# Performance work log

Hardware: AMD Instinct MI355X
Metric: run time of the kernel (lower is better)

Reference implementation:

```python
import jax, jax.numpy as jnp
import numpy as np

B, S, H, E = 4, 4096, 2048, 16
ED = H // 4
LN_EPS = 1e-5
ROUTING_SCALE = 0.01
NEG_INF = -1e9


def setup_inputs() -> dict:
    key = jax.random.key(0)
    ks = jax.random.split(key, 10)
    std = 0.02
    w_std = 1.0 / np.sqrt(H)  # roughly nn.Linear default scale
    return {
        "hidden_states": jax.random.normal(ks[0], (B, S, H), jnp.float32),
        "layer_embeddings": jax.random.normal(ks[1], (E, H), jnp.float32) * std,
        "centrality_embeddings": jax.random.normal(ks[2], (E, H), jnp.float32) * std,
        "spatial_embeddings": jax.random.normal(ks[3], (E + 1, 1), jnp.float32) * std,
        "edge_embeddings": jax.random.normal(ks[4], (E, ED), jnp.float32) * std,
        "ln_gamma": jnp.ones((H,), jnp.float32),
        "ln_beta": jnp.zeros((H,), jnp.float32),
        "Wq": jax.random.normal(ks[5], (H, H), jnp.float32) * w_std,
        "bq": jnp.zeros((H,), jnp.float32),
        "Wk": jax.random.normal(ks[6], (H, H), jnp.float32) * w_std,
        "bk": jnp.zeros((H,), jnp.float32),
        "Wv": jax.random.normal(ks[7], (H, H), jnp.float32) * w_std,
        "bv": jnp.zeros((H,), jnp.float32),
        "current_layer": 0,  # current_depth == 0 path: used_experts = {0}
        "available_mask": jnp.ones((E,), jnp.int32).at[0].set(0),
    }


def _layer_norm(x, g, b):
    mu = jnp.mean(x, axis=-1, keepdims=True)
    var = jnp.mean(jnp.square(x - mu), axis=-1, keepdims=True)
    return (x - mu) * jax.lax.rsqrt(var + LN_EPS) * g + b


def reference(hidden_states, layer_embeddings, centrality_embeddings,
              spatial_embeddings, edge_embeddings, ln_gamma, ln_beta,
              Wq, bq, Wk, bk, Wv, bv, current_layer, available_mask):
    avail = available_mask.astype(jnp.float32)  # [E]

    # --- attention scores over experts ---
    current_embed = layer_embeddings[current_layer]                 # [H]
    normed = _layer_norm(hidden_states, ln_gamma, ln_beta)          # [B,S,H]
    hidden_mean = jnp.mean(normed, axis=1)                          # [B,H]
    query_input = current_embed + hidden_mean                       # [B,H]
    layer_features = layer_embeddings + centrality_embeddings       # [E,H]

    q = query_input @ Wq.T + bq                                     # [B,H]
    k = layer_features @ Wk.T + bk                                  # [E,H]
    # v is computed in the original but never used downstream of scores
    _v = layer_features @ Wv.T + bv                                 # [E,H]

    attention = (q @ k.T) / np.sqrt(H)                              # [B,E]

    # --- spatial bias ---
    idx = jnp.arange(E)
    distances = jnp.abs(idx - current_layer)                        # [E]
    spatial_bias = spatial_embeddings[distances, 0]                 # [E]

    # --- edge bias: vectorized form of the per-expert loop ---
    # sum over i in available, i != current: (edge_emb[i] @ edge_emb.T) / max(dist_i,1)
    ew = edge_embeddings @ edge_embeddings.T                        # [E,E]
    scale = 1.0 / jnp.maximum(distances, 1).astype(jnp.float32)     # [E]
    row_mask = avail * (idx != current_layer).astype(jnp.float32)   # [E]
    edge_bias = jnp.einsum("i,ij->j", row_mask * scale, ew)         # [E]

    scores = attention + spatial_bias + edge_bias                   # [B,E]
    scores = jnp.where(avail > 0, scores, NEG_INF)                  # mask unavailable

    # --- routing loss (KL to uniform-over-available, batchmean) ---
    probs = jax.nn.softmax(scores, axis=-1)                         # [B,E]
    num_avail = jnp.sum(avail)
    t = 1.0 / num_avail                                             # scalar target prob
    probs_safe = jnp.clip(probs, 1e-10)
    kl = jnp.sum(t * (jnp.log(t) - jnp.log(probs_safe))) / B
    routing_loss = kl * ROUTING_SCALE

    next_idx = jnp.argmax(probs[0], axis=-1)
    return routing_loss, probs, next_idx
```

## Files before the change

### kernel.cpp

```cpp
#include <hip/hip_runtime.h>
#include <hip/hip_bf16.h>

#define DEV __device__ __forceinline__

constexpr float INV_SQRT_H = 0.022097086912079608f;

constexpr size_t WS_PART = 0;
constexpr size_t WS_MU   = WS_PART + (size_t)1024 * 2048;
constexpr size_t WS_QI   = WS_MU + 4096;
constexpr size_t WS_Q    = WS_QI + 4 * 2048;
constexpr size_t WS_K    = WS_Q + 4 * 2048;

DEV bool is_bf16_probe(const void* g) {
    return ((const unsigned int*)g)[0] == 0x3F803F80u;
}

template <bool BF16>
DEV void load8(const void* base, size_t idx, float* o) {
    if constexpr (BF16) {
        const unsigned short* p = (const unsigned short*)base + idx;
        uint4 u = *(const uint4*)p;
        o[0] = __uint_as_float(u.x << 16); o[1] = __uint_as_float(u.x & 0xFFFF0000u);
        o[2] = __uint_as_float(u.y << 16); o[3] = __uint_as_float(u.y & 0xFFFF0000u);
        o[4] = __uint_as_float(u.z << 16); o[5] = __uint_as_float(u.z & 0xFFFF0000u);
        o[6] = __uint_as_float(u.w << 16); o[7] = __uint_as_float(u.w & 0xFFFF0000u);
    } else {
        const float* p = (const float*)base + idx;
        float4 a = *(const float4*)p;
        float4 b = *(const float4*)(p + 4);
        o[0] = a.x; o[1] = a.y; o[2] = a.z; o[3] = a.w;
        o[4] = b.x; o[5] = b.y; o[6] = b.z; o[7] = b.w;
    }
}

template <bool BF16>
DEV float ld1(const void* base, size_t idx) {
    if constexpr (BF16) {
        unsigned int v = ((const unsigned short*)base)[idx];
        return __uint_as_float(v << 16);
    } else {
        return ((const float*)base)[idx];
    }
}

template <bool BF16>
DEV void st1(void* base, size_t idx, float v) {
    if constexpr (BF16) {
        ((__hip_bfloat16*)base)[idx] = __float2bfloat16(v);
    } else {
        ((float*)base)[idx] = v;
    }
}

template <bool BF16>
DEV void kA_body(const void* hidden, const void* lemb, const void* cemb,
                 const void* Wk, const void* bk, float* ws) {
    int bid = blockIdx.x;
    int wave = threadIdx.x >> 6, lane = threadIdx.x & 63;

    if (bid < 1024) {
        int b = bid >> 8;
        int chunk = bid & 255;

        float acc[32];
#pragma unroll
        for (int i = 0; i < 32; ++i) acc[i] = 0.f;
        float accmu = 0.f;

        for (int r = 0; r < 4; ++r) {
            int s = chunk * 16 + wave * 4 + r;
            size_t base = ((size_t)(b * 4096 + s)) * 2048;
            float x[32];
#pragma unroll
            for (int j = 0; j < 4; ++j)
                load8<BF16>(hidden, base + j * 512 + lane * 8, &x[j * 8]);
            float s1 = 0.f, s2 = 0.f;
#pragma unroll
            for (int i = 0; i < 32; ++i) { s1 += x[i]; s2 += x[i] * x[i]; }
#pragma unroll
            for (int off = 1; off < 64; off <<= 1) {
                s1 += __shfl_xor(s1, off);
                s2 += __shfl_xor(s2, off);
            }
            float mu = s1 * (1.f / 2048.f);
            float var = s2 * (1.f / 2048.f) - mu * mu;
            float rsig = rsqrtf(var + 1e-5f);
            accmu += rsig * mu;
#pragma unroll
            for (int i = 0; i < 32; ++i) acc[i] += rsig * x[i];
        }

        __shared__ float lds[4 * 2048];
#pragma unroll
        for (int j = 0; j < 4; ++j) {
            float4 v0 = make_float4(acc[j * 8 + 0], acc[j * 8 + 1], acc[j * 8 + 2], acc[j * 8 + 3]);
            float4 v1 = make_float4(acc[j * 8 + 4], acc[j * 8 + 5], acc[j * 8 + 6], acc[j * 8 + 7]);
            *(float4*)&lds[wave * 2048 + j * 512 + lane * 8 + 0] = v0;
            *(float4*)&lds[wave * 2048 + j * 512 + lane * 8 + 4] = v1;
        }
        __syncthreads();
        int c0 = threadIdx.x * 8;
        float4 s0, s1v;
        s0.x = lds[0 * 2048 + c0 + 0] + lds[1 * 2048 + c0 + 0] + lds[2 * 2048 + c0 + 0] + lds[3 * 2048 + c0 + 0];
        s0.y = lds[0 * 2048 + c0 + 1] + lds[1 * 2048 + c0 + 1] + lds[2 * 2048 + c0 + 1] + lds[3 * 2048 + c0 + 1];
        s0.z = lds[0 * 2048 + c0 + 2] + lds[1 * 2048 + c0 + 2] + lds[2 * 2048 + c0 + 2] + lds[3 * 2048 + c0 + 2];
        s0.w = lds[0 * 2048 + c0 + 3] + lds[1 * 2048 + c0 + 3] + lds[2 * 2048 + c0 + 3] + lds[3 * 2048 + c0 + 3];
        s1v.x = lds[0 * 2048 + c0 + 4] + lds[1 * 2048 + c0 + 4] + lds[2 * 2048 + c0 + 4] + lds[3 * 2048 + c0 + 4];
        s1v.y = lds[0 * 2048 + c0 + 5] + lds[1 * 2048 + c0 + 5] + lds[2 * 2048 + c0 + 5] + lds[3 * 2048 + c0 + 5];
        s1v.z = lds[0 * 2048 + c0 + 6] + lds[1 * 2048 + c0 + 6] + lds[2 * 2048 + c0 + 6] + lds[3 * 2048 + c0 + 6];
        s1v.w = lds[0 * 2048 + c0 + 7] + lds[1 * 2048 + c0 + 7] + lds[2 * 2048 + c0 + 7] + lds[3 * 2048 + c0 + 7];
        float* part = ws + WS_PART + (size_t)bid * 2048 + c0;
        *(float4*)(part + 0) = s0;
        *(float4*)(part + 4) = s1v;
        if (lane == 0) ws[WS_MU + bid * 4 + wave] = accmu;
    } else {
        int h = (bid - 1024) * 4 + wave;
        float acc[16];
#pragma unroll
        for (int e = 0; e < 16; ++e) acc[e] = 0.f;
#pragma unroll
        for (int ci = 0; ci < 4; ++ci) {
            int c0 = ci * 512 + lane * 8;
            float w8[8];
            load8<BF16>(Wk, (size_t)h * 2048 + c0, w8);
#pragma unroll
            for (int e = 0; e < 16; ++e) {
                float l8[8], c8[8];
                load8<BF16>(lemb, (size_t)e * 2048 + c0, l8);
                load8<BF16>(cemb, (size_t)e * 2048 + c0, c8);
#pragma unroll
                for (int j = 0; j < 8; ++j) acc[e] += w8[j] * (l8[j] + c8[j]);
            }
        }
#pragma unroll
        for (int e = 0; e < 16; ++e)
#pragma unroll
            for (int off = 1; off < 64; off <<= 1) acc[e] += __shfl_xor(acc[e], off);
        if (lane == 0) {
            float bias = ld1<BF16>(bk, h);
#pragma unroll
            for (int e = 0; e < 16; ++e) ws[WS_K + (size_t)e * 2048 + h] = acc[e] + bias;
        }
    }
}

__global__ __launch_bounds__(256) void kA(const void* hidden, const void* lemb,
                                          const void* cemb, const void* Wk,
                                          const void* bk, const void* probe, float* ws) {
    if (is_bf16_probe(probe)) kA_body<true>(hidden, lemb, cemb, Wk, bk, ws);
    else kA_body<false>(hidden, lemb, cemb, Wk, bk, ws);
}

template <bool BF16>
DEV void kB_body(float* ws, const void* gamma, const void* beta, const void* lemb,
                 const int* curp) {
    int bid = blockIdx.x, tid = threadIdx.x;
    int b = bid >> 4, cc = bid & 15;
    __shared__ float smu[4];
    __shared__ float comb[128];
    float m = ws[WS_MU + b * 1024 + tid] + ws[WS_MU + b * 1024 + 256 + tid] +
              ws[WS_MU + b * 1024 + 512 + tid] + ws[WS_MU + b * 1024 + 768 + tid];
#pragma unroll
    for (int off = 1; off < 64; off <<= 1) m += __shfl_xor(m, off);
    if ((tid & 63) == 0) smu[tid >> 6] = m;
    int col = cc * 128 + (tid & 127);
    int p0 = (tid < 128) ? 0 : 128;
    float a = 0.f;
#pragma unroll 4
    for (int p = p0; p < p0 + 128; ++p)
        a += ws[WS_PART + ((size_t)(b * 256 + p)) * 2048 + col];
    if (tid >= 128) comb[tid - 128] = a;
    __syncthreads();
    if (tid < 128) {
        float accmu = smu[0] + smu[1] + smu[2] + smu[3];
        float tot = a + comb[tid];
        float hm = ld1<BF16>(gamma, col) * (tot - accmu) * (1.f / 4096.f) +
                   ld1<BF16>(beta, col);
        int cur = curp[0];
        ws[WS_QI + b * 2048 + col] = ld1<BF16>(lemb, (size_t)cur * 2048 + col) + hm;
    }
}

__global__ __launch_bounds__(256) void kB(float* ws, const void* gamma, const void* beta,
                                          const void* lemb, const int* curp) {
    if (is_bf16_probe(gamma)) kB_body<true>(ws, gamma, beta, lemb, curp);
    else kB_body<false>(ws, gamma, beta, lemb, curp);
}

template <bool BF16>
DEV void kC_body(float* ws, const void* Wq, const void* bq) {
    int bid = blockIdx.x;
    int wave = threadIdx.x >> 6, lane = threadIdx.x & 63;
    int h = bid * 4 + wave;
    float acc[4];
#pragma unroll
    for (int b = 0; b < 4; ++b) acc[b] = 0.f;
#pragma unroll
    for (int ci = 0; ci < 4; ++ci) {
        int c0 = ci * 512 + lane * 8;
        float w8[8];
        load8<BF16>(Wq, (size_t)h * 2048 + c0, w8);
#pragma unroll
        for (int b = 0; b < 4; ++b) {
            const float* qi = ws + WS_QI + (size_t)b * 2048 + c0;
            float4 u1 = *(const float4*)qi;
            float4 u2 = *(const float4*)(qi + 4);
            acc[b] += w8[0] * u1.x + w8[1] * u1.y + w8[2] * u1.z + w8[3] * u1.w +
                      w8[4] * u2.x + w8[5] * u2.y + w8[6] * u2.z + w8[7] * u2.w;
        }
    }
#pragma unroll
    for (int b = 0; b < 4; ++b)
#pragma unroll
        for (int off = 1; off < 64; off <<= 1) acc[b] += __shfl_xor(acc[b], off);
    if (lane == 0) {
        float bias = ld1<BF16>(bq, h);
#pragma unroll
        for (int b = 0; b < 4; ++b) ws[WS_Q + (size_t)b * 2048 + h] = acc[b] + bias;
    }
}

__global__ __launch_bounds__(256) void kC(float* ws, const void* Wq, const void* bq,
                                          const void* probe) {
    if (is_bf16_probe(probe)) kC_body<true>(ws, Wq, bq);
    else kC_body<false>(ws, Wq, bq);
}

template <bool BF16>
DEV void kD_body(float* ws, const void* spat, const void* edge, const int* curp,
                 const int* availp, void* out) {
    __shared__ float att[64];
    int wave = threadIdx.x >> 6, lane64 = threadIdx.x & 63;
    int b = wave;

    float q[32];
#pragma unroll
    for (int ci = 0; ci < 4; ++ci) {
        const float* qp = ws + WS_Q + (size_t)b * 2048 + ci * 512 + lane64 * 8;
        float4 a = *(const float4*)qp;
        float4 c = *(const float4*)(qp + 4);
        q[ci * 8 + 0] = a.x; q[ci * 8 + 1] = a.y; q[ci * 8 + 2] = a.z; q[ci * 8 + 3] = a.w;
        q[ci * 8 + 4] = c.x; q[ci * 8 + 5] = c.y; q[ci * 8 + 6] = c.z; q[ci * 8 + 7] = c.w;
    }
    for (int e = 0; e < 16; ++e) {
        float acc = 0.f;
#pragma unroll
        for (int ci = 0; ci < 4; ++ci) {
            const float* kp = ws + WS_K + (size_t)e * 2048 + ci * 512 + lane64 * 8;
            float4 x1 = *(const float4*)kp;
            float4 x2 = *(const float4*)(kp + 4);
            acc += q[ci * 8 + 0] * x1.x + q[ci * 8 + 1] * x1.y +
                   q[ci * 8 + 2] * x1.z + q[ci * 8 + 3] * x1.w +
                   q[ci * 8 + 4] * x2.x + q[ci * 8 + 5] * x2.y +
                   q[ci * 8 + 6] * x2.z + q[ci * 8 + 7] * x2.w;
        }
#pragma unroll
        for (int off = 1; off < 64; off <<= 1) acc += __shfl_xor(acc, off);
        if (lane64 == 0) att[b * 16 + e] = acc * INV_SQRT_H;
    }
    __syncthreads();
    if (wave != 0) return;

    int lane = lane64;
    int cur = curp[0];
    int av[16];
    int navail = 0;
#pragma unroll
    for (int i = 0; i < 16; ++i) { av[i] = availp[i]; navail += (av[i] != 0); }

    int d0 = lane * 8;
    float w8[8];
#pragma unroll
    for (int qq = 0; qq < 8; ++qq) w8[qq] = 0.f;
    for (int i = 0; i < 16; ++i) {
        if (av[i] && i != cur) {
            int dist = i > cur ? i - cur : cur - i;
            float coef = 1.f / (float)(dist > 1 ? dist : 1);
            float e8[8];
            load8<BF16>(edge, (size_t)i * 512 + d0, e8);
#pragma unroll
            for (int qq = 0; qq < 8; ++qq) w8[qq] += coef * e8[qq];
        }
    }
    float bias[16];
    for (int j = 0; j < 16; ++j) {
        float e8[8];
        load8<BF16>(edge, (size_t)j * 512 + d0, e8);
        float p = w8[0] * e8[0] + w8[1] * e8[1] + w8[2] * e8[2] + w8[3] * e8[3] +
                  w8[4] * e8[4] + w8[5] * e8[5] + w8[6] * e8[6] + w8[7] * e8[7];
#pragma unroll
        for (int off = 1; off < 64; off <<= 1) p += __shfl_xor(p, off);
        bias[j] = p;
    }

    int e = lane & 15;
    int dist_e = e > cur ? e - cur : cur - e;
    float sp = ld1<BF16>(spat, dist_e);
    float s = att[lane] + sp + bias[e];
    if (!av[e]) s = -1e9f;

    float m = s;
#pragma unroll
    for (int off = 1; off < 16; off <<= 1) m = fmaxf(m, __shfl_xor(m, off));
    float ex = expf(s - m);
    float sum = ex;
#pragma unroll
    for (int off = 1; off < 16; off <<= 1) sum += __shfl_xor(sum, off);
    float p = ex / sum;
    st1<BF16>(out, 1 + lane, p);

    float t = 1.f / (float)navail;
    float term = t * (logf(t) - logf(fmaxf(p, 1e-10f)));
    float tot = term;
#pragma unroll
    for (int off = 1; off < 64; off <<= 1) tot += __shfl_xor(tot, off);
    if (lane == 0) st1<BF16>(out, 0, tot * (0.01f / 4.f));

    float m2 = p;
#pragma unroll
    for (int off = 1; off < 16; off <<= 1) m2 = fmaxf(m2, __shfl_xor(m2, off));
    int cand = (p == m2 && lane < 16) ? e : 1000;
#pragma unroll
    for (int off = 1; off < 16; off <<= 1) cand = min(cand, __shfl_xor(cand, off));
    if (lane == 0) st1<BF16>(out, 65, (float)cand);
}

__global__ __launch_bounds__(256) void kD(float* ws, const void* spat, const void* edge,
                                          const void* probe, const int* curp,
                                          const int* availp, void* out) {
    if (is_bf16_probe(probe)) kD_body<true>(ws, spat, edge, curp, availp, out);
    else kD_body<false>(ws, spat, edge, curp, availp, out);
}

extern "C" void kernel_launch(void* const* d_in, const int* in_sizes, int n_in,
                              void* d_out, int out_size, void* d_ws, size_t ws_size,
                              hipStream_t stream) {
    const void* hidden = d_in[0];
    const void* lemb   = d_in[1];
    const void* cemb   = d_in[2];
    const void* spat   = d_in[3];
    const void* edge   = d_in[4];
    const void* gamma  = d_in[5];
    const void* beta   = d_in[6];
    const void* Wq     = d_in[7];
    const void* bq     = d_in[8];
    const void* Wk     = d_in[9];
    const void* bk     = d_in[10];
    const int* curp    = (const int*)d_in[13];
    const int* availp  = (const int*)d_in[14];
    float* ws = (float*)d_ws;

    kA<<<1536, 256, 0, stream>>>(hidden, lemb, cemb, Wk, bk, gamma, ws);
    kB<<<64, 256, 0, stream>>>(ws, gamma, beta, lemb, curp);
    kC<<<512, 256, 0, stream>>>(ws, Wq, bq, gamma);
    kD<<<1, 256, 0, stream>>>(ws, spat, edge, gamma, curp, availp, d_out);
}
```

Before: 297.6 us.

## Write per-wave partial sums directly and widen kB reduction grid

kA no longer reduces its four waves' partial column sums through shared memory with a block barrier. Each wave now writes its own 2048-float partial to the workspace, which makes the partial buffer four times larger. kB is relaunched with 256 blocks of 32 columns each, split into 8 row groups, so the larger partial buffer is reduced with more parallelism. The change removes the LDS traffic and barrier in kA, but adds roughly 3x more workspace write and read traffic (about 64 MB versus 16 MB).

```diff
diff --git a/kernel.cpp b/kernel.cpp
--- a/kernel.cpp
+++ b/kernel.cpp
@@ -6,7 +6,7 @@
 constexpr float INV_SQRT_H = 0.022097086912079608f;
 
 constexpr size_t WS_PART = 0;
-constexpr size_t WS_MU   = WS_PART + (size_t)1024 * 2048;
+constexpr size_t WS_MU   = WS_PART + (size_t)4096 * 2048;
 constexpr size_t WS_QI   = WS_MU + 4096;
 constexpr size_t WS_Q    = WS_QI + 4 * 2048;
 constexpr size_t WS_K    = WS_Q + 4 * 2048;
@@ -61,6 +61,7 @@
     if (bid < 1024) {
         int b = bid >> 8;
         int chunk = bid & 255;
+        int pid = bid * 4 + wave;
 
         float acc[32];
 #pragma unroll
@@ -90,29 +91,15 @@
             for (int i = 0; i < 32; ++i) acc[i] += rsig * x[i];
         }
 
-        __shared__ float lds[4 * 2048];
+        float* part = ws + WS_PART + (size_t)pid * 2048;
 #pragma unroll
         for (int j = 0; j < 4; ++j) {
             float4 v0 = make_float4(acc[j * 8 + 0], acc[j * 8 + 1], acc[j * 8 + 2], acc[j * 8 + 3]);
             float4 v1 = make_float4(acc[j * 8 + 4], acc[j * 8 + 5], acc[j * 8 + 6], acc[j * 8 + 7]);
-            *(float4*)&lds[wave * 2048 + j * 512 + lane * 8 + 0] = v0;
-            *(float4*)&lds[wave * 2048 + j * 512 + lane * 8 + 4] = v1;
-        }
-        __syncthreads();
-        int c0 = threadIdx.x * 8;
-        float4 s0, s1v;
-        s0.x = lds[0 * 2048 + c0 + 0] + lds[1 * 2048 + c0 + 0] + lds[2 * 2048 + c0 + 0] + lds[3 * 2048 + c0 + 0];
-        s0.y = lds[0 * 2048 + c0 + 1] + lds[1 * 2048 + c0 + 1] + lds[2 * 2048 + c0 + 1] + lds[3 * 2048 + c0 + 1];
-        s0.z = lds[0 * 2048 + c0 + 2] + lds[1 * 2048 + c0 + 2] + lds[2 * 2048 + c0 + 2] + lds[3 * 2048 + c0 + 2];
-        s0.w = lds[0 * 2048 + c0 + 3] + lds[1 * 2048 + c0 + 3] + lds[2 * 2048 + c0 + 3] + lds[3 * 2048 + c0 + 3];
-        s1v.x = lds[0 * 2048 + c0 + 4] + lds[1 * 2048 + c0 + 4] + lds[2 * 2048 + c0 + 4] + lds[3 * 2048 + c0 + 4];
-        s1v.y = lds[0 * 2048 + c0 + 5] + lds[1 * 2048 + c0 + 5] + lds[2 * 2048 + c0 + 5] + lds[3 * 2048 + c0 + 5];
-        s1v.z = lds[0 * 2048 + c0 + 6] + lds[1 * 2048 + c0 + 6] + lds[2 * 2048 + c0 + 6] + lds[3 * 2048 + c0 + 6];
-        s1v.w = lds[0 * 2048 + c0 + 7] + lds[1 * 2048 + c0 + 7] + lds[2 * 2048 + c0 + 7] + lds[3 * 2048 + c0 + 7];
-        float* part = ws + WS_PART + (size_t)bid * 2048 + c0;
-        *(float4*)(part + 0) = s0;
-        *(float4*)(part + 4) = s1v;
-        if (lane == 0) ws[WS_MU + bid * 4 + wave] = accmu;
+            *(float4*)(part + j * 512 + lane * 8 + 0) = v0;
+            *(float4*)(part + j * 512 + lane * 8 + 4) = v1;
+        }
+        if (lane == 0) ws[WS_MU + pid] = accmu;
     } else {
         int h = (bid - 1024) * 4 + wave;
         float acc[16];
@@ -155,29 +142,33 @@
 DEV void kB_body(float* ws, const void* gamma, const void* beta, const void* lemb,
                  const int* curp) {
     int bid = blockIdx.x, tid = threadIdx.x;
-    int b = bid >> 4, cc = bid & 15;
+    int b = bid >> 6, cc = bid & 63;
     __shared__ float smu[4];
-    __shared__ float comb[128];
-    float m = ws[WS_MU + b * 1024 + tid] + ws[WS_MU + b * 1024 + 256 + tid] +
-              ws[WS_MU + b * 1024 + 512 + tid] + ws[WS_MU + b * 1024 + 768 + tid];
+    __shared__ float comb[8][32];
+
+    float4 mv = *(const float4*)(ws + WS_MU + (size_t)b * 1024 + tid * 4);
+    float m = mv.x + mv.y + mv.z + mv.w;
 #pragma unroll
     for (int off = 1; off < 64; off <<= 1) m += __shfl_xor(m, off);
     if ((tid & 63) == 0) smu[tid >> 6] = m;
-    int col = cc * 128 + (tid & 127);
-    int p0 = (tid < 128) ? 0 : 128;
+
+    int col = cc * 32 + (tid & 31);
+    int pg = tid >> 5;
     float a = 0.f;
 #pragma unroll 4
-    for (int p = p0; p < p0 + 128; ++p)
-        a += ws[WS_PART + ((size_t)(b * 256 + p)) * 2048 + col];
-    if (tid >= 128) comb[tid - 128] = a;
+    for (int p = pg * 128; p < pg * 128 + 128; ++p)
+        a += ws[WS_PART + ((size_t)(b * 1024 + p)) * 2048 + col];
+    comb[pg][tid & 31] = a;
     __syncthreads();
-    if (tid < 128) {
+    if (tid < 32) {
         float accmu = smu[0] + smu[1] + smu[2] + smu[3];
-        float tot = a + comb[tid];
-        float hm = ld1<BF16>(gamma, col) * (tot - accmu) * (1.f / 4096.f) +
-                   ld1<BF16>(beta, col);
+        float tot = comb[0][tid] + comb[1][tid] + comb[2][tid] + comb[3][tid] +
+                    comb[4][tid] + comb[5][tid] + comb[6][tid] + comb[7][tid];
+        int c = cc * 32 + tid;
+        float hm = ld1<BF16>(gamma, c) * (tot - accmu) * (1.f / 4096.f) +
+                   ld1<BF16>(beta, c);
         int cur = curp[0];
-        ws[WS_QI + b * 2048 + col] = ld1<BF16>(lemb, (size_t)cur * 2048 + col) + hm;
+        ws[WS_QI + b * 2048 + c] = ld1<BF16>(lemb, (size_t)cur * 2048 + c) + hm;
     }
 }
 
@@ -351,7 +342,7 @@
     float* ws = (float*)d_ws;
 
     kA<<<1536, 256, 0, stream>>>(hidden, lemb, cemb, Wk, bk, gamma, ws);
-    kB<<<64, 256, 0, stream>>>(ws, gamma, beta, lemb, curp);
+    kB<<<256, 256, 0, stream>>>(ws, gamma, beta, lemb, curp);
     kC<<<512, 256, 0, stream>>>(ws, Wq, bq, gamma);
     kD<<<1, 256, 0, stream>>>(ws, spat, edge, gamma, curp, availp, d_out);
 }
```

New measurement: 306.5 us. 1.03x slower.
